# Kernel optimization log

Measured on AMD Instinct MI355X. Metric: run time of the kernel, lower is better.

The kernel has to match this reference:

```python
import jax, jax.numpy as jnp
import numpy as np

S, B, D, H = 4096, 4, 1024, 16
DH = D // H


def _xavier(key, fan_in, fan_out):
    bound = float(np.sqrt(6.0 / (fan_in + fan_out)))
    return jax.random.uniform(key, (fan_out, fan_in), jnp.float32, -bound, bound)


def setup_inputs() -> dict:
    key = jax.random.key(0)
    kq, kk, kv, kwq, kwk, kwv = jax.random.split(key, 6)
    return {
        "q": jax.random.normal(kq, (S, B, D), jnp.float32),
        "k": jax.random.normal(kk, (S, B, D), jnp.float32),
        "v": jax.random.normal(kv, (S, B, D), jnp.float32),
        "Wq": _xavier(kwq, D, D),
        "Wk": _xavier(kwk, D, D),
        "Wv": _xavier(kwv, D, D),
    }


def reference(q, k, v, Wq, Wk, Wv):
    s, b = q.shape[:2]
    # exp feature maps after bias-free linear projections (nn.Linear: x @ W.T)
    q_h = jnp.exp(q @ Wq.T).reshape(s, b, H, DH)
    k_h = jnp.exp(k @ Wk.T).reshape(s, b, H, DH)
    v_h = (v @ Wv.T).reshape(s, b, H, DH)
    # original: einsum('sbnd,sbnde->sbne', q, k[...,None]*v[None...]) / same-with-ones
    # contract over d without materializing the (s,b,n,d,e) outer product
    qk = jnp.einsum('sbnd,sbnd->sbn', q_h, k_h)[..., None]  # (s,b,n,1)
    out = (qk * v_h) / qk                                   # (s,b,n,dh)
    out = out.reshape(s, b, D)
    return jnp.cumsum(out, axis=1)  # cumsum over dim=1 (batch), as in source
```

## Files before the change

### kernel.cpp

```cpp
#include <hip/hip_runtime.h>
#include <hip/hip_bf16.h>


typedef short s16x8 __attribute__((ext_vector_type(8)));
typedef float f32x4 __attribute__((ext_vector_type(4)));

constexpr int M_ = 16384, N_ = 1024, K_ = 1024;
constexpr int KT = 16;
constexpr size_t WS_WB   = 33554432;
constexpr size_t WS_NEED = 35651584;

static __device__ __forceinline__ unsigned cvtpk(float lo, float hi) {
  unsigned r;
  asm("v_cvt_pk_bf16_f32 %0, %1, %2" : "=v"(r) : "v"(lo), "v"(hi));
  return r;
}

__global__ __launch_bounds__(256) void cvt_bf16(const float* __restrict__ v,
                                                const float* __restrict__ w,
                                                unsigned short* __restrict__ vb,
                                                unsigned short* __restrict__ wb) {
  const int gs = gridDim.x * blockDim.x;
  const int t0 = blockIdx.x * blockDim.x + threadIdx.x;
  for (int i = t0; i < (M_ * K_ / 4); i += gs) {
    float4 x = ((const float4*)v)[i];
    uint2 p; p.x = cvtpk(x.x, x.y); p.y = cvtpk(x.z, x.w);
    ((uint2*)vb)[i] = p;
  }
  for (int i = t0; i < (N_ * K_ / 4); i += gs) {
    float4 x = ((const float4*)w)[i];
    uint2 p; p.x = cvtpk(x.x, x.y); p.y = cvtpk(x.z, x.w);
    ((uint2*)wb)[i] = p;
  }
}

#define GLL(srcp, ldsoff)                                                     \
  __builtin_amdgcn_global_load_lds(                                           \
      (__attribute__((address_space(1))) void*)(void*)(srcp),                 \
      (__attribute__((address_space(3))) void*)(void*)(lds + (ldsoff)),       \
      16, 0, 0)

#define SB() __builtin_amdgcn_sched_barrier(0)

#define MFMA_Q(MB, AF, BF)                                                    \
  __builtin_amdgcn_s_setprio(1);                                              \
  _Pragma("unroll") for (int m_ = 0; m_ < 4; ++m_)                            \
  _Pragma("unroll") for (int n_ = 0; n_ < 4; ++n_)                            \
      acc[(MB) + m_][n_] = __builtin_amdgcn_mfma_f32_16x16x32_bf16(           \
          AF[m_], BF[n_], acc[(MB) + m_][n_], 0, 0, 0);                       \
  __builtin_amdgcn_s_setprio(0);

__global__ __launch_bounds__(512, 2) void la_gemm8(
    const unsigned short* __restrict__ Ab,
    const unsigned short* __restrict__ Bb,
    float* __restrict__ out) {
  extern __shared__ char lds[];

  const int tid = threadIdx.x, lane = tid & 63, wave = tid >> 6;
  const int wr = wave >> 2, wc = wave & 3;

  const int gid = blockIdx.x;
  const int xcd = gid & 7, qq = gid >> 3;
  const int mt = xcd * 8 + (qq >> 2), nt = qq & 3;

  const int l3 = lane >> 3, l7 = lane & 7;
  const int sch = ((l7 ^ l3) << 4);
  const char* sA[2][2]; const char* sB[2][2];
#pragma unroll
  for (int h = 0; h < 2; ++h)
#pragma unroll
    for (int j = 0; j < 2; ++j) {
      const size_t ar = (size_t)(mt * 256 + h * 128 + j * 64 + wave * 8 + l3);
      const size_t br = (size_t)(nt * 256 + h * 128 + j * 64 + wave * 8 + l3);
      sA[h][j] = (const char*)Ab + ar * 2048 + sch;
      sB[h][j] = (const char*)Bb + br * 2048 + sch;
    }
  const int ldsw = wave * 1024;

  const int basa = wr * 16384 + (lane & 15) * 128 + (((lane >> 4) ^ l7) << 4);
  const int basb = 32768 + (wc >> 1) * 16384 +
                   ((wc & 1) * 64 + (lane & 15)) * 128 + (((lane >> 4) ^ l7) << 4);

  f32x4 acc[8][4] = {};

  GLL(sA[0][0], 0 + ldsw);             GLL(sA[0][1], 8192 + ldsw);
  GLL(sA[1][0], 16384 + ldsw);         GLL(sA[1][1], 24576 + ldsw);
  GLL(sB[0][0], 32768 + ldsw);         GLL(sB[0][1], 40960 + ldsw);
  GLL(sB[1][0], 49152 + ldsw);         GLL(sB[1][1], 57344 + ldsw);
  asm volatile("s_waitcnt vmcnt(0)" ::: "memory");
  __syncthreads();

  for (int kt = 0; kt < KT; ++kt) {
    const int cb = (kt & 1) << 16;
    const int nb = cb ^ 65536;
    const int ko = (kt + 1) * 128;
    const bool pf = (kt + 1 < KT);

    s16x8 af[4], ag[4], bf0[4], bf1[4];

#pragma unroll
    for (int n = 0; n < 4; ++n) bf0[n] = *(const s16x8*)(lds + cb + basb + n * 2048);
#pragma unroll
    for (int m = 0; m < 4; ++m) af[m] = *(const s16x8*)(lds + cb + basa + m * 2048);
#pragma unroll
    for (int m = 0; m < 4; ++m) ag[m] = *(const s16x8*)(lds + cb + basa + (4 + m) * 2048);
    if (pf) {
      GLL(sA[0][0] + ko, nb + 0     + ldsw);  GLL(sA[0][1] + ko, nb + 8192  + ldsw);
      GLL(sA[1][0] + ko, nb + 16384 + ldsw);  GLL(sA[1][1] + ko, nb + 24576 + ldsw);
    }
    SB();
    MFMA_Q(0, af, bf0);
    SB();

#pragma unroll
    for (int n = 0; n < 4; ++n) bf1[n] = *(const s16x8*)(lds + cb + ((basb + n * 2048) ^ 64));
#pragma unroll
    for (int m = 0; m < 4; ++m) af[m] = *(const s16x8*)(lds + cb + ((basa + m * 2048) ^ 64));
    if (pf) {
      GLL(sB[0][0] + ko, nb + 32768 + ldsw);  GLL(sB[0][1] + ko, nb + 40960 + ldsw);
      GLL(sB[1][0] + ko, nb + 49152 + ldsw);  GLL(sB[1][1] + ko, nb + 57344 + ldsw);
    }
    SB();
    MFMA_Q(4, ag, bf0);
    SB();

#pragma unroll
    for (int m = 0; m < 4; ++m) ag[m] = *(const s16x8*)(lds + cb + ((basa + (4 + m) * 2048) ^ 64));
    SB();
    MFMA_Q(0, af, bf1);
    SB();
    MFMA_Q(4, ag, bf1);
    SB();

    asm volatile("s_waitcnt vmcnt(0)" ::: "memory");
    __builtin_amdgcn_s_barrier();
  }

#pragma unroll
  for (int m = 0; m < 8; ++m) {
    const int row0 = mt * 256 + wr * 128 + m * 16 + ((lane >> 4) << 2);
#pragma unroll
    for (int n = 0; n < 4; ++n) {
      f32x4 a = acc[m][n];
      a.y += a.x;  a.z += a.y;  a.w += a.z;
      const int col = nt * 256 + wc * 64 + n * 16 + (lane & 15);
      out[(size_t)(row0 + 0) * N_ + col] = a.x;
      out[(size_t)(row0 + 1) * N_ + col] = a.y;
      out[(size_t)(row0 + 2) * N_ + col] = a.z;
      out[(size_t)(row0 + 3) * N_ + col] = a.w;
    }
  }
}

__global__ __launch_bounds__(512, 2) void la_gemm_fb(
    const float* __restrict__ Vp, const float* __restrict__ Wp, float* __restrict__ out) {
  extern __shared__ char lds[];
  const int tid = threadIdx.x, lane = tid & 63, wave = tid >> 6;
  const int wr = wave >> 2, wc = wave & 3;
  const int gid = blockIdx.x, xcd = gid & 7, q = gid >> 3;
  const int mt = xcd * 8 + (q >> 2), nt = q & 3;
  const int srow = tid >> 3, schunk = tid & 7;
  const float* sAp = Vp + (size_t)(mt * 256 + srow) * K_ + schunk * 8;
  const float* sBp = Wp + (size_t)(nt * 256 + srow) * K_ + schunk * 8;
  const int wbyte = srow * 128 + ((schunk ^ (srow & 7)) << 4);
  const int basa0 = (wr * 128 + (lane & 15)) * 128 + (((lane >> 4) ^ (lane & 7)) << 4);
  const int basb0 = (wc * 64 + (lane & 15)) * 128 + (((lane >> 4) ^ (lane & 7)) << 4);
  f32x4 acc[8][4] = {};
  float4 sa[8], sb[8];
  auto loadset = [&](int kt) {
#pragma unroll
    for (int i = 0; i < 4; ++i) {
      const float* pa = sAp + kt * 64 + i * (64 * K_);
      const float* pb = sBp + kt * 64 + i * (64 * K_);
      sa[2*i] = *(const float4*)pa; sa[2*i+1] = *(const float4*)(pa + 4);
      sb[2*i] = *(const float4*)pb; sb[2*i+1] = *(const float4*)(pb + 4);
    }
  };
  auto cvtwrite = [&](int buf) {
    char* A = lds + buf * 65536; char* B = A + 32768;
#pragma unroll
    for (int i = 0; i < 4; ++i) {
      uint4 wa, wb;
      wa.x = cvtpk(sa[2*i].x, sa[2*i].y);     wa.y = cvtpk(sa[2*i].z, sa[2*i].w);
      wa.z = cvtpk(sa[2*i+1].x, sa[2*i+1].y); wa.w = cvtpk(sa[2*i+1].z, sa[2*i+1].w);
      wb.x = cvtpk(sb[2*i].x, sb[2*i].y);     wb.y = cvtpk(sb[2*i].z, sb[2*i].w);
      wb.z = cvtpk(sb[2*i+1].x, sb[2*i+1].y); wb.w = cvtpk(sb[2*i+1].z, sb[2*i+1].w);
      *(uint4*)(A + wbyte + i * 8192) = wa;
      *(uint4*)(B + wbyte + i * 8192) = wb;
    }
  };
  auto compute = [&](int buf) {
    const char* A = lds + buf * 65536; const char* B = A + 32768;
#pragma unroll
    for (int kk = 0; kk < 2; ++kk) {
      const int ba = basa0 ^ (kk ? 64 : 0), bb = basb0 ^ (kk ? 64 : 0);
      s16x8 bf[4];
#pragma unroll
      for (int n = 0; n < 4; ++n) bf[n] = *(const s16x8*)(B + bb + n * 2048);
#pragma unroll
      for (int mh = 0; mh < 2; ++mh) {
        s16x8 af[4];
#pragma unroll
        for (int m = 0; m < 4; ++m) af[m] = *(const s16x8*)(A + ba + (mh * 4 + m) * 2048);
        __builtin_amdgcn_s_setprio(1);
#pragma unroll
        for (int m = 0; m < 4; ++m)
#pragma unroll
          for (int n = 0; n < 4; ++n)
            acc[mh*4+m][n] = __builtin_amdgcn_mfma_f32_16x16x32_bf16(af[m], bf[n], acc[mh*4+m][n], 0, 0, 0);
        __builtin_amdgcn_s_setprio(0);
      }
    }
  };
  loadset(0); cvtwrite(0); __syncthreads();
  for (int kt = 0; kt < KT; ++kt) {
    const int cur = kt & 1;
    if (kt + 1 < KT) loadset(kt + 1);
    compute(cur);
    if (kt + 1 < KT) cvtwrite(cur ^ 1);
    __syncthreads();
  }
#pragma unroll
  for (int m = 0; m < 8; ++m) {
    const int row0 = mt * 256 + wr * 128 + m * 16 + ((lane >> 4) << 2);
#pragma unroll
    for (int n = 0; n < 4; ++n) {
      f32x4 a = acc[m][n];
      a.y += a.x; a.z += a.y; a.w += a.z;
      const int col = nt * 256 + wc * 64 + n * 16 + (lane & 15);
      out[(size_t)(row0 + 0) * N_ + col] = a.x;
      out[(size_t)(row0 + 1) * N_ + col] = a.y;
      out[(size_t)(row0 + 2) * N_ + col] = a.z;
      out[(size_t)(row0 + 3) * N_ + col] = a.w;
    }
  }
}

extern "C" void kernel_launch(void* const* d_in, const int* in_sizes, int n_in,
                              void* d_out, int out_size, void* d_ws, size_t ws_size,
                              hipStream_t stream) {
  const float* v  = (const float*)d_in[2];
  const float* Wv = (const float*)d_in[5];
  float* out = (float*)d_out;
  (void)in_sizes; (void)n_in; (void)out_size;

  if (ws_size >= WS_NEED) {
    unsigned short* vb = (unsigned short*)d_ws;
    unsigned short* wb = (unsigned short*)((char*)d_ws + WS_WB);
    cvt_bf16<<<dim3(2048), dim3(256), 0, stream>>>(v, Wv, vb, wb);
    hipFuncSetAttribute((const void*)la_gemm8,
                        hipFuncAttributeMaxDynamicSharedMemorySize, 131072);
    la_gemm8<<<dim3(256), dim3(512), 131072, stream>>>(vb, wb, out);
  } else {
    hipFuncSetAttribute((const void*)la_gemm_fb,
                        hipFuncAttributeMaxDynamicSharedMemorySize, 131072);
    la_gemm_fb<<<dim3(256), dim3(512), 131072, stream>>>(v, Wv, out);
  }
}
```

Baseline: 55.24 us.

## Restructure bf16 GEMM main loop into 4-stage LDS pipeline with 64-wide K tiles

Replaces the double-buffered 128-wide K tile loop with a four-buffer ring of 64-wide K tiles, prefetching three tiles ahead and waiting with partial vmcnt counts instead of draining all loads each iteration. The LDS layout and XOR swizzle change to match the narrower tiles, and explicit s_barriers are placed around MFMA groups to keep waves in lockstep. The aim is to hide global-to-LDS latency behind more in-flight loads. The cost is twice as many iterations, extra barriers per tile, and a tail that is unrolled by hand.

```diff
diff --git a/kernel.cpp b/kernel.cpp
--- a/kernel.cpp
+++ b/kernel.cpp
@@ -6,7 +6,7 @@
 typedef float f32x4 __attribute__((ext_vector_type(4)));
 
 constexpr int M_ = 16384, N_ = 1024, K_ = 1024;
-constexpr int KT = 16;
+constexpr int KT32 = 32;
 constexpr size_t WS_WB   = 33554432;
 constexpr size_t WS_NEED = 35651584;
 
@@ -41,6 +41,7 @@
       16, 0, 0)
 
 #define SB() __builtin_amdgcn_sched_barrier(0)
+#define VMNT(n) asm volatile("s_waitcnt vmcnt(" #n ")" ::: "memory")
 
 #define MFMA_Q(MB, AF, BF)                                                    \
   __builtin_amdgcn_s_setprio(1);                                              \
@@ -50,6 +51,33 @@
           AF[m_], BF[n_], acc[(MB) + m_][n_], 0, 0, 0);                       \
   __builtin_amdgcn_s_setprio(0);
 
+#define TILE_BODY(KT, PF, VMWAIT) do {                                        \
+    const int ktv_ = (KT);                                                    \
+    const char* Rb_ = lds + ((ktv_ & 3) << 15);                               \
+    const int sb_ = (((ktv_ + 3) & 3) << 15);                                 \
+    const int ko_ = (ktv_ + 3) * 64;                                          \
+    s16x8 bf[4], af[4], ag[4];                                                \
+                               \
+    _Pragma("unroll") for (int n_ = 0; n_ < 4; ++n_)                          \
+      bf[n_] = *(const s16x8*)(Rb_ + RB + n_ * 1024);                         \
+    _Pragma("unroll") for (int m_ = 0; m_ < 4; ++m_)                          \
+      af[m_] = *(const s16x8*)(Rb_ + RA + m_ * 1024);                         \
+    if (PF) { GLL(srcA0 + ko_, sb_ + ldsA0); GLL(srcA1 + ko_, sb_ + ldsA1); } \
+    SB();                                                                     \
+    __builtin_amdgcn_s_barrier();                                             \
+    MFMA_Q(0, af, bf);                                                        \
+    __builtin_amdgcn_s_barrier();                                             \
+       \
+    _Pragma("unroll") for (int m_ = 0; m_ < 4; ++m_)                          \
+      ag[m_] = *(const s16x8*)(Rb_ + RA + (4 + m_) * 1024);                   \
+    if (PF) { GLL(srcB0 + ko_, sb_ + ldsB0); GLL(srcB1 + ko_, sb_ + ldsB1); } \
+    SB();                                                                     \
+    __builtin_amdgcn_s_barrier();                                             \
+    MFMA_Q(4, ag, bf);                                                        \
+    VMWAIT;                                                                   \
+    __builtin_amdgcn_s_barrier();                                             \
+  } while (0)
+
 __global__ __launch_bounds__(512, 2) void la_gemm8(
     const unsigned short* __restrict__ Ab,
     const unsigned short* __restrict__ Bb,
@@ -63,78 +91,35 @@
   const int xcd = gid & 7, qq = gid >> 3;
   const int mt = xcd * 8 + (qq >> 2), nt = qq & 3;
 
-  const int l3 = lane >> 3, l7 = lane & 7;
-  const int sch = ((l7 ^ l3) << 4);
-  const char* sA[2][2]; const char* sB[2][2];
-#pragma unroll
-  for (int h = 0; h < 2; ++h)
-#pragma unroll
-    for (int j = 0; j < 2; ++j) {
-      const size_t ar = (size_t)(mt * 256 + h * 128 + j * 64 + wave * 8 + l3);
-      const size_t br = (size_t)(nt * 256 + h * 128 + j * 64 + wave * 8 + l3);
-      sA[h][j] = (const char*)Ab + ar * 2048 + sch;
-      sB[h][j] = (const char*)Bb + br * 2048 + sch;
-    }
-  const int ldsw = wave * 1024;
-
-  const int basa = wr * 16384 + (lane & 15) * 128 + (((lane >> 4) ^ l7) << 4);
-  const int basb = 32768 + (wc >> 1) * 16384 +
-                   ((wc & 1) * 64 + (lane & 15)) * 128 + (((lane >> 4) ^ l7) << 4);
+  const int l15 = lane & 15;
+  const int lswz = (((lane >> 4) ^ ((l15 >> 1) & 3)) << 4);
+  const int RA = (wr * 128 + l15) * 64 + lswz;
+  const int RB = 16384 + (wc * 64 + l15) * 64 + lswz;
+
+  const int cg = ((lane & 3) ^ ((lane >> 3) & 3)) << 4;
+  const int u0 = 2 * wave, u1 = 2 * wave + 1;
+  const char* srcA0 = (const char*)Ab + (size_t)(mt * 256 + u0 * 16 + (lane >> 2)) * 2048 + cg;
+  const char* srcA1 = (const char*)Ab + (size_t)(mt * 256 + u1 * 16 + (lane >> 2)) * 2048 + cg;
+  const char* srcB0 = (const char*)Bb + (size_t)(nt * 256 + u0 * 16 + (lane >> 2)) * 2048 + cg;
+  const char* srcB1 = (const char*)Bb + (size_t)(nt * 256 + u1 * 16 + (lane >> 2)) * 2048 + cg;
+  const int ldsA0 = u0 * 1024, ldsA1 = u1 * 1024;
+  const int ldsB0 = 16384 + u0 * 1024, ldsB1 = 16384 + u1 * 1024;
 
   f32x4 acc[8][4] = {};
 
-  GLL(sA[0][0], 0 + ldsw);             GLL(sA[0][1], 8192 + ldsw);
-  GLL(sA[1][0], 16384 + ldsw);         GLL(sA[1][1], 24576 + ldsw);
-  GLL(sB[0][0], 32768 + ldsw);         GLL(sB[0][1], 40960 + ldsw);
-  GLL(sB[1][0], 49152 + ldsw);         GLL(sB[1][1], 57344 + ldsw);
-  asm volatile("s_waitcnt vmcnt(0)" ::: "memory");
+#pragma unroll
+  for (int t = 0; t < 3; ++t) {
+    const int sb = t << 15, ko = t * 64;
+    GLL(srcA0 + ko, sb + ldsA0); GLL(srcA1 + ko, sb + ldsA1);
+    GLL(srcB0 + ko, sb + ldsB0); GLL(srcB1 + ko, sb + ldsB1);
+  }
+  VMNT(8);
   __syncthreads();
 
-  for (int kt = 0; kt < KT; ++kt) {
-    const int cb = (kt & 1) << 16;
-    const int nb = cb ^ 65536;
-    const int ko = (kt + 1) * 128;
-    const bool pf = (kt + 1 < KT);
-
-    s16x8 af[4], ag[4], bf0[4], bf1[4];
-
-#pragma unroll
-    for (int n = 0; n < 4; ++n) bf0[n] = *(const s16x8*)(lds + cb + basb + n * 2048);
-#pragma unroll
-    for (int m = 0; m < 4; ++m) af[m] = *(const s16x8*)(lds + cb + basa + m * 2048);
-#pragma unroll
-    for (int m = 0; m < 4; ++m) ag[m] = *(const s16x8*)(lds + cb + basa + (4 + m) * 2048);
-    if (pf) {
-      GLL(sA[0][0] + ko, nb + 0     + ldsw);  GLL(sA[0][1] + ko, nb + 8192  + ldsw);
-      GLL(sA[1][0] + ko, nb + 16384 + ldsw);  GLL(sA[1][1] + ko, nb + 24576 + ldsw);
-    }
-    SB();
-    MFMA_Q(0, af, bf0);
-    SB();
-
-#pragma unroll
-    for (int n = 0; n < 4; ++n) bf1[n] = *(const s16x8*)(lds + cb + ((basb + n * 2048) ^ 64));
-#pragma unroll
-    for (int m = 0; m < 4; ++m) af[m] = *(const s16x8*)(lds + cb + ((basa + m * 2048) ^ 64));
-    if (pf) {
-      GLL(sB[0][0] + ko, nb + 32768 + ldsw);  GLL(sB[0][1] + ko, nb + 40960 + ldsw);
-      GLL(sB[1][0] + ko, nb + 49152 + ldsw);  GLL(sB[1][1] + ko, nb + 57344 + ldsw);
-    }
-    SB();
-    MFMA_Q(4, ag, bf0);
-    SB();
-
-#pragma unroll
-    for (int m = 0; m < 4; ++m) ag[m] = *(const s16x8*)(lds + cb + ((basa + (4 + m) * 2048) ^ 64));
-    SB();
-    MFMA_Q(0, af, bf1);
-    SB();
-    MFMA_Q(4, ag, bf1);
-    SB();
-
-    asm volatile("s_waitcnt vmcnt(0)" ::: "memory");
-    __builtin_amdgcn_s_barrier();
-  }
+  for (int kt = 0; kt < 29; ++kt) TILE_BODY(kt, true, VMNT(8));
+  TILE_BODY(29, false, VMNT(4));
+  TILE_BODY(30, false, VMNT(0));
+  TILE_BODY(31, false, (void)0);
 
 #pragma unroll
   for (int m = 0; m < 8; ++m) {
@@ -143,7 +128,7 @@
     for (int n = 0; n < 4; ++n) {
       f32x4 a = acc[m][n];
       a.y += a.x;  a.z += a.y;  a.w += a.z;
-      const int col = nt * 256 + wc * 64 + n * 16 + (lane & 15);
+      const int col = nt * 256 + wc * 64 + n * 16 + l15;
       out[(size_t)(row0 + 0) * N_ + col] = a.x;
       out[(size_t)(row0 + 1) * N_ + col] = a.y;
       out[(size_t)(row0 + 2) * N_ + col] = a.z;
@@ -213,11 +198,11 @@
     }
   };
   loadset(0); cvtwrite(0); __syncthreads();
-  for (int kt = 0; kt < KT; ++kt) {
+  for (int kt = 0; kt < 16; ++kt) {
     const int cur = kt & 1;
-    if (kt + 1 < KT) loadset(kt + 1);
+    if (kt + 1 < 16) loadset(kt + 1);
     compute(cur);
-    if (kt + 1 < KT) cvtwrite(cur ^ 1);
+    if (kt + 1 < 16) cvtwrite(cur ^ 1);
     __syncthreads();
   }
 #pragma unroll
```

Measured after the change: 59.03 us. +6.9%, slower.
